# Kernel tuning notes

Measured on AMD Instinct MI355X. Metric: run time of the kernel, lower is better.

## Reference

```python
import jax, jax.numpy as jnp
import numpy as np
from jax import lax

FACTOR = 2  # fixed down-sampling factor in StyleGAN2 conv_downsample_2d
RESAMPLE_KERNEL = [1, 3, 3, 1]


def _setup_kernel(k):
    # StyleGAN2 _setup_kernel: separable 1D -> 2D outer product, normalized to sum 1
    k = np.asarray(k, dtype=np.float32)
    if k.ndim == 1:
        k = np.outer(k, k)
    k /= k.sum()
    return k


def setup_inputs() -> dict:
    key = jax.random.key(0)
    k1, k2 = jax.random.split(key)
    images = jax.random.normal(k1, (4, 128, 512, 512), dtype=jnp.float32)  # NCHW
    # equalised_weights: use_w_scale=True, lr_mult=1 -> init_std = 1.0; runtime_coeff
    # is computed in build() but never applied in call(), so weights are used raw.
    w = jax.random.normal(k2, (1, 1, 128, 256), dtype=jnp.float32)  # HWIO [kh,kw,inC,outC]
    return {"images": images, "w": w}


def reference(images, w):
    # conv_downsample_2d(x, w, k=[1,3,3,1], factor=2, gain=1), NCHW:
    #   k2d = setup(k) * gain
    #   p = (len2d(k) - factor) + (convW - 1); pad0=(p+1)//2, pad1=p//2
    #   x = upfirdn2d(x, k2d, up=1, down=1, pad0, pad1)  # per-channel FIR
    #   out = conv2d(x, w, strides=factor, padding='VALID')
    k2d = _setup_kernel(RESAMPLE_KERNEL)  # [4,4], gain=1
    kh = k2d.shape[0]
    convw = w.shape[1]
    p = (kh - FACTOR) + (convw - 1)
    pad0, pad1 = (p + 1) // 2, p // 2

    C = images.shape[1]
    # upfirdn applies true convolution with k2d == correlation with spatially flipped k2d
    fir = jnp.asarray(k2d[::-1, ::-1])[:, :, None, None]          # [kh,kw,1,1]
    fir = jnp.broadcast_to(fir, (kh, kh, 1, C)).astype(images.dtype)  # depthwise HWIO
    x = lax.conv_general_dilated(
        images, fir,
        window_strides=(1, 1),
        padding=[(pad0, pad1), (pad0, pad1)],
        dimension_numbers=("NCHW", "HWIO", "NCHW"),
        feature_group_count=C,
    )
    out = lax.conv_general_dilated(
        x, w,
        window_strides=(FACTOR, FACTOR),
        padding="VALID",
        dimension_numbers=("NCHW", "HWIO", "NCHW"),
    )
    return out  # [4, 256, 256, 256]
```

## Files before the change

### kernel.cpp

```cpp
#include <hip/hip_runtime.h>


#define CH    8
#define RPIT  35
#define CSTR  631
#define YPIT  144

typedef __attribute__((ext_vector_type(4))) float f32x4;

__device__ __forceinline__ int yoff(int g) { return g * 8 + ((g >> 2) << 2); }

__global__ __launch_bounds__(512)
void fused_downconv_f32v6(const float* __restrict__ x, const float* __restrict__ w,
                          float* __restrict__ out) {
    __shared__ __align__(16) float x_s[CH * CSTR];
    __shared__ __align__(16) float y_s[CH * YPIT];

    const int tid  = threadIdx.x;
    const int lane = tid & 63;
    const int wv   = tid >> 6;

    const int oc_g = tid >> 4;
    const int sp_g = tid & 15;

    const int ow0 = blockIdx.x * 16;
    const int oh0 = blockIdx.y * 8;
    const int n   = blockIdx.z;

    const int rbase = 2 * oh0 - 1;
    const int cbase = 2 * ow0 - 1;

    int off[10];
    unsigned ldmask = 0;
    unsigned wrapmask = 0;
    int la0;
    {
        int row = (lane >= 34) ? 1 : 0;
        int col = lane - (row ? 34 : 0);
        la0 = wv * CSTR + row * RPIT + col;
        #pragma unroll
        for (int k = 0; k < 10; k++) {
            bool have = (k < 9) || (lane < 36);
            int gr = rbase + row, gc = cbase + col;
            bool ok = have && ((unsigned)gr < 512u) && ((unsigned)gc < 512u);
            off[k] = ok ? (gr * 512 + gc) : 0;
            if (ok) ldmask |= (1u << k);
            int c2 = col + 30;
            bool wr = (c2 >= 34);
            if (wr) wrapmask |= (1u << k);
            col = wr ? (c2 - 34) : c2;
            row += wr ? 2 : 1;
        }
    }
    const unsigned stmask = (lane < 36) ? 0x3FFu : 0x1FFu;

    float xr[10];
    f32x4 accA[8], accB[8];
    #pragma unroll
    for (int i = 0; i < 8; i++) {
        accA[i] = (f32x4){0.f, 0.f, 0.f, 0.f};
        accB[i] = (f32x4){0.f, 0.f, 0.f, 0.f};
    }

    auto do_prefetch = [&](int c0) {
        const float* xb = x + ((size_t)(n * 128 + c0 + wv)) * 262144;
        #pragma unroll
        for (int k = 0; k < 10; k++)
            xr[k] = ((ldmask >> k) & 1u) ? xb[off[k]] : 0.f;
    };

    do_prefetch(0);

    const int yp_xb  = wv * CSTR + (lane >> 3) * (2 * RPIT) + (lane & 7) * 4;
    const int yp_sp  = (lane >> 3) * 16 + (lane & 7) * 2;
    const int yp_dst = wv * YPIT + yoff(yp_sp >> 3) + (yp_sp & 7);
    const int y_rd   = yoff(sp_g);

    for (int c0 = 0; c0 < 128; c0 += CH) {
        {
            int la = la0;
            #pragma unroll
            for (int k = 0; k < 10; k++) {
                if ((stmask >> k) & 1u) x_s[la] = xr[k];
                la += ((wrapmask >> k) & 1u) ? 66 : 65;
            }
        }
        __syncthreads();

        if (c0 + CH < 128) do_prefetch(c0 + CH);

        {
            const float* xb = &x_s[yp_xb];
            float colv[6];
            #pragma unroll
            for (int j = 0; j < 6; j++)
                colv[j] = 0.125f * (xb[j] + xb[3 * RPIT + j])
                        + 0.375f * (xb[RPIT + j] + xb[2 * RPIT + j]);
            float y0 = 0.125f * (colv[0] + colv[3]) + 0.375f * (colv[1] + colv[2]);
            float y1 = 0.125f * (colv[2] + colv[5]) + 0.375f * (colv[3] + colv[4]);
            *(float2*)&y_s[yp_dst] = make_float2(y0, y1);
        }
        __syncthreads();

        {
            const float* wp = w + (size_t)c0 * 256 + oc_g * 8;
            #pragma unroll
            for (int cc = 0; cc < CH; cc++) {
                f32x4 wa = *(const f32x4*)&wp[cc * 256];
                f32x4 wb = *(const f32x4*)&wp[cc * 256 + 4];
                f32x4 ya = *(const f32x4*)&y_s[cc * YPIT + y_rd];
                f32x4 yb = *(const f32x4*)&y_s[cc * YPIT + y_rd + 4];
                accA[0] += wa.x * ya;  accB[0] += wa.x * yb;
                accA[1] += wa.y * ya;  accB[1] += wa.y * yb;
                accA[2] += wa.z * ya;  accB[2] += wa.z * yb;
                accA[3] += wa.w * ya;  accB[3] += wa.w * yb;
                accA[4] += wb.x * ya;  accB[4] += wb.x * yb;
                accA[5] += wb.y * ya;  accB[5] += wb.y * yb;
                accA[6] += wb.z * ya;  accB[6] += wb.z * yb;
                accA[7] += wb.w * ya;  accB[7] += wb.w * yb;
            }
        }
    }

    {
        const int oh_l = sp_g >> 1;
        const int owst = (sp_g & 1) * 8;
        const size_t obase = (((size_t)n * 256 + (size_t)oc_g * 8) * 256
                              + (size_t)(oh0 + oh_l)) * 256 + ow0 + owst;
        #pragma unroll
        for (int i = 0; i < 8; i++) {
            *(f32x4*)&out[obase + (size_t)i * 65536]     = accA[i];
            *(f32x4*)&out[obase + (size_t)i * 65536 + 4] = accB[i];
        }
    }
}

extern "C" void kernel_launch(void* const* d_in, const int* in_sizes, int n_in,
                              void* d_out, int out_size, void* d_ws, size_t ws_size,
                              hipStream_t stream) {
    const float* x = (const float*)d_in[0];
    const float* w = (const float*)d_in[1];
    float* out = (float*)d_out;

    dim3 grid(16, 32, 4);
    dim3 block(512);
    hipLaunchKernelGGL(fused_downconv_f32v6, grid, block, 0, stream, x, w, out);
}
```

Before: 430.1 us.

## Restructure fused downsample-conv with register vertical FIR and double-buffered LDS

Rewrites the kernel so each lane loads a column of 10 input rows and applies the vertical FIR in registers, writing vertically filtered rows into a double-buffered LDS array, then applies the horizontal FIR at read time. Each wave owns 32 output channels with scalar (wave-uniform) weight loads and per-thread scalar accumulators, and the output tile shrinks to 4x16, doubling the grid. Double buffering removes one barrier per channel chunk and overlaps the next chunk's global loads and vertical filtering with the channel-reduction math. In exchange, halving the output rows per block raises the overlap of input rows re-read between neighbouring blocks, and output stores become scalar instead of vectorised.

```diff
diff --git a/kernel.cpp b/kernel.cpp
--- a/kernel.cpp
+++ b/kernel.cpp
@@ -1,30 +1,20 @@
 #include <hip/hip_runtime.h>
 
 
-#define CH    8
-#define RPIT  35
-#define CSTR  631
-#define YPIT  144
-
-typedef __attribute__((ext_vector_type(4))) float f32x4;
-
-__device__ __forceinline__ int yoff(int g) { return g * 8 + ((g >> 2) << 2); }
+#define VS 35
 
 __global__ __launch_bounds__(512)
-void fused_downconv_f32v6(const float* __restrict__ x, const float* __restrict__ w,
-                          float* __restrict__ out) {
-    __shared__ __align__(16) float x_s[CH * CSTR];
-    __shared__ __align__(16) float y_s[CH * YPIT];
+void fused_downconv_v7(const float* __restrict__ x, const float* __restrict__ w,
+                       float* __restrict__ out) {
+    __shared__ __align__(16) float v_s[2 * 8 * 4 * VS];
 
     const int tid  = threadIdx.x;
     const int lane = tid & 63;
     const int wv   = tid >> 6;
-
-    const int oc_g = tid >> 4;
-    const int sp_g = tid & 15;
+    const int oc0  = __builtin_amdgcn_readfirstlane((tid >> 6) << 5);
 
     const int ow0 = blockIdx.x * 16;
-    const int oh0 = blockIdx.y * 8;
+    const int oh0 = blockIdx.y * 4;
     const int n   = blockIdx.z;
 
     const int rbase = 2 * oh0 - 1;
@@ -32,106 +22,73 @@
 
     int off[10];
     unsigned ldmask = 0;
-    unsigned wrapmask = 0;
-    int la0;
     {
-        int row = (lane >= 34) ? 1 : 0;
-        int col = lane - (row ? 34 : 0);
-        la0 = wv * CSTR + row * RPIT + col;
+        int gc = cbase + lane;
+        bool cok = (lane < 34) && ((unsigned)gc < 512u);
         #pragma unroll
         for (int k = 0; k < 10; k++) {
-            bool have = (k < 9) || (lane < 36);
-            int gr = rbase + row, gc = cbase + col;
-            bool ok = have && ((unsigned)gr < 512u) && ((unsigned)gc < 512u);
+            int gr = rbase + k;
+            bool ok = cok && ((unsigned)gr < 512u);
             off[k] = ok ? (gr * 512 + gc) : 0;
-            if (ok) ldmask |= (1u << k);
-            int c2 = col + 30;
-            bool wr = (c2 >= 34);
-            if (wr) wrapmask |= (1u << k);
-            col = wr ? (c2 - 34) : c2;
-            row += wr ? 2 : 1;
+            if (ok) ldmask |= 1u << k;
         }
     }
-    const unsigned stmask = (lane < 36) ? 0x3FFu : 0x1FFu;
+
+    const int owl = lane & 15;
+    const int ohl = lane >> 4;
 
     float xr[10];
-    f32x4 accA[8], accB[8];
+    float acc[32];
     #pragma unroll
-    for (int i = 0; i < 8; i++) {
-        accA[i] = (f32x4){0.f, 0.f, 0.f, 0.f};
-        accB[i] = (f32x4){0.f, 0.f, 0.f, 0.f};
-    }
+    for (int i = 0; i < 32; i++) acc[i] = 0.f;
 
-    auto do_prefetch = [&](int c0) {
+    auto prefetch = [&](int c0) {
         const float* xb = x + ((size_t)(n * 128 + c0 + wv)) * 262144;
         #pragma unroll
         for (int k = 0; k < 10; k++)
             xr[k] = ((ldmask >> k) & 1u) ? xb[off[k]] : 0.f;
     };
-
-    do_prefetch(0);
-
-    const int yp_xb  = wv * CSTR + (lane >> 3) * (2 * RPIT) + (lane & 7) * 4;
-    const int yp_sp  = (lane >> 3) * 16 + (lane & 7) * 2;
-    const int yp_dst = wv * YPIT + yoff(yp_sp >> 3) + (yp_sp & 7);
-    const int y_rd   = yoff(sp_g);
-
-    for (int c0 = 0; c0 < 128; c0 += CH) {
-        {
-            int la = la0;
+    auto vwrite = [&](int buf) {
+        if (lane < 34) {
             #pragma unroll
-            for (int k = 0; k < 10; k++) {
-                if ((stmask >> k) & 1u) x_s[la] = xr[k];
-                la += ((wrapmask >> k) & 1u) ? 66 : 65;
+            for (int o = 0; o < 4; o++) {
+                float v = 0.125f * (xr[2 * o] + xr[2 * o + 3])
+                        + 0.375f * (xr[2 * o + 1] + xr[2 * o + 2]);
+                v_s[((buf * 8 + wv) * 4 + o) * VS + lane] = v;
             }
         }
-        __syncthreads();
+    };
 
-        if (c0 + CH < 128) do_prefetch(c0 + CH);
+    prefetch(0);
+    vwrite(0);
+    prefetch(8);
+    __syncthreads();
 
-        {
-            const float* xb = &x_s[yp_xb];
-            float colv[6];
+    for (int t = 0; t < 16; t++) {
+        const int buf = t & 1;
+        if (t < 15) {
+            vwrite(buf ^ 1);
+            if (t < 14) prefetch((t + 2) * 8);
+        }
+        #pragma unroll
+        for (int cc = 0; cc < 8; cc++) {
+            const float* vp = &v_s[((buf * 8 + cc) * 4 + ohl) * VS + 2 * owl];
+            float v0 = vp[0], v1 = vp[1], v2 = vp[2], v3 = vp[3];
+            float y = 0.125f * (v0 + v3) + 0.375f * (v1 + v2);
+            const float* wrow = w + ((t * 8 + cc) << 8) + oc0;
             #pragma unroll
-            for (int j = 0; j < 6; j++)
-                colv[j] = 0.125f * (xb[j] + xb[3 * RPIT + j])
-                        + 0.375f * (xb[RPIT + j] + xb[2 * RPIT + j]);
-            float y0 = 0.125f * (colv[0] + colv[3]) + 0.375f * (colv[1] + colv[2]);
-            float y1 = 0.125f * (colv[2] + colv[5]) + 0.375f * (colv[3] + colv[4]);
-            *(float2*)&y_s[yp_dst] = make_float2(y0, y1);
+            for (int i = 0; i < 32; i++)
+                acc[i] = fmaf(wrow[i], y, acc[i]);
         }
         __syncthreads();
-
-        {
-            const float* wp = w + (size_t)c0 * 256 + oc_g * 8;
-            #pragma unroll
-            for (int cc = 0; cc < CH; cc++) {
-                f32x4 wa = *(const f32x4*)&wp[cc * 256];
-                f32x4 wb = *(const f32x4*)&wp[cc * 256 + 4];
-                f32x4 ya = *(const f32x4*)&y_s[cc * YPIT + y_rd];
-                f32x4 yb = *(const f32x4*)&y_s[cc * YPIT + y_rd + 4];
-                accA[0] += wa.x * ya;  accB[0] += wa.x * yb;
-                accA[1] += wa.y * ya;  accB[1] += wa.y * yb;
-                accA[2] += wa.z * ya;  accB[2] += wa.z * yb;
-                accA[3] += wa.w * ya;  accB[3] += wa.w * yb;
-                accA[4] += wb.x * ya;  accB[4] += wb.x * yb;
-                accA[5] += wb.y * ya;  accB[5] += wb.y * yb;
-                accA[6] += wb.z * ya;  accB[6] += wb.z * yb;
-                accA[7] += wb.w * ya;  accB[7] += wb.w * yb;
-            }
-        }
     }
 
     {
-        const int oh_l = sp_g >> 1;
-        const int owst = (sp_g & 1) * 8;
-        const size_t obase = (((size_t)n * 256 + (size_t)oc_g * 8) * 256
-                              + (size_t)(oh0 + oh_l)) * 256 + ow0 + owst;
+        size_t base = (((size_t)n * 256 + oc0) * 256 + (size_t)(oh0 + ohl)) * 256
+                      + ow0 + owl;
         #pragma unroll
-        for (int i = 0; i < 8; i++) {
-            *(f32x4*)&out[obase + (size_t)i * 65536]     = accA[i];
-            *(f32x4*)&out[obase + (size_t)i * 65536 + 4] = accB[i];
-        }
+        for (int i = 0; i < 32; i++)
+            out[base + (size_t)i * 65536] = acc[i];
     }
 }
 
@@ -142,7 +99,7 @@
     const float* w = (const float*)d_in[1];
     float* out = (float*)d_out;
 
-    dim3 grid(16, 32, 4);
+    dim3 grid(16, 64, 4);
     dim3 block(512);
-    hipLaunchKernelGGL(fused_downconv_f32v6, grid, block, 0, stream, x, w, out);
+    hipLaunchKernelGGL(fused_downconv_v7, grid, block, 0, stream, x, w, out);
 }
```

After: 411.7 us. 1.04x faster.
